# Optimization experiments

Measured on AMD Instinct MI355X. Metric: run time of the kernel, lower is better.

Reference implementation:

```python
import jax, jax.numpy as jnp
import numpy as np

N = 40000   # num nodes
C = 128     # in_channels
H = 8       # num_heads
D = C // H  # head_dim = 16
E = 640000  # num edges
FF = 4 * C


def layer_norm(x, g, b, eps=1e-5):
    m = jnp.mean(x, axis=-1, keepdims=True)
    v = jnp.mean((x - m) ** 2, axis=-1, keepdims=True)
    return (x - m) / jnp.sqrt(v + eps) * g + b


def setup_inputs() -> dict:
    key = jax.random.key(0)
    ks = jax.random.split(key, 16)
    s = 0.02
    x = jax.random.normal(ks[0], (N, C), dtype=jnp.float32)
    edge_index = jax.random.randint(ks[1], (2, E), 0, N, dtype=jnp.int64)
    return {
        'x': x,
        'edge_index': edge_index,
        'Wq': jax.random.normal(ks[2], (C, C), jnp.float32) * s,
        'bq': jnp.zeros((C,), jnp.float32),
        'Wk': jax.random.normal(ks[3], (C, C), jnp.float32) * s,
        'bk': jnp.zeros((C,), jnp.float32),
        'Wv': jax.random.normal(ks[4], (C, C), jnp.float32) * s,
        'bv': jnp.zeros((C,), jnp.float32),
        'Wo': jax.random.normal(ks[5], (C, C), jnp.float32) * s,
        'bo': jnp.zeros((C,), jnp.float32),
        'ln1_g': jnp.ones((C,), jnp.float32),
        'ln1_b': jnp.zeros((C,), jnp.float32),
        'ln2_g': jnp.ones((C,), jnp.float32),
        'ln2_b': jnp.zeros((C,), jnp.float32),
        'W1': jax.random.normal(ks[6], (C, FF), jnp.float32) * s,
        'b1': jnp.zeros((FF,), jnp.float32),
        'W2': jax.random.normal(ks[7], (FF, C), jnp.float32) * s,
        'b2': jnp.zeros((C,), jnp.float32),
    }


def reference(x, edge_index, Wq, bq, Wk, bk, Wv, bv, Wo, bo,
              ln1_g, ln1_b, ln2_g, ln2_b, W1, b1, W2, b2):
    residual = x
    xn = layer_norm(x, ln1_g, ln1_b)
    q = (xn @ Wq + bq).reshape(N, H, D)
    k = (xn @ Wk + bk).reshape(N, H, D)
    v = (xn @ Wv + bv).reshape(N, H, D)
    src, dst = edge_index[0], edge_index[1]
    # per-edge scores: [E, H]
    scores = jnp.einsum('ehd,ehd->eh', q[dst], k[src]) / jnp.sqrt(jnp.float32(D))
    # NOTE: faithful to the source — softmax over ALL edges (dim=0), not per-destination
    attn = jax.nn.softmax(scores, axis=0)[:, :, None]          # [E, H, 1]
    weighted = v[src] * attn                                   # [E, H, D]
    aggregated = jax.ops.segment_sum(weighted, dst, num_segments=N)  # [N, H, D]
    out = aggregated.reshape(N, C) @ Wo + bo
    x1 = residual + out
    residual2 = x1
    xn2 = layer_norm(x1, ln2_g, ln2_b)
    ffn = jax.nn.relu(xn2 @ W1 + b1) @ W2 + b2
    return residual2 + ffn
```

## Files before the change

kernel.cpp:

```cpp
#include <hip/hip_runtime.h>
#include <math.h>

#define NNODES 40000
#define CCH    128
#define NH     8
#define HD     16
#define NEDGE  640000
#define NBLK   157
#define FBLK   10000
#define RBLK   40
#define EBLK   625

typedef __attribute__((ext_vector_type(8))) short bf16x8;
typedef __attribute__((ext_vector_type(4))) float f32x4;
typedef __attribute__((ext_vector_type(2))) float f32x2;

__device__ inline unsigned short f2bf(float f) {
  union { float f; unsigned u; } c; c.f = f;
  unsigned r = c.u + 0x7fffu + ((c.u >> 16) & 1u);
  return (unsigned short)(r >> 16);
}
__device__ inline float bfs(unsigned short u) { union { unsigned i; float f; } c; c.i = (unsigned)u << 16; return c.f; }
__device__ inline float bflo(unsigned u) { union { unsigned i; float f; } c; c.i = u << 16; return c.f; }
__device__ inline float bfhi(unsigned u) { union { unsigned i; float f; } c; c.i = u & 0xffff0000u; return c.f; }

__device__ inline unsigned char f2fp8(float v) {
#if __has_builtin(__builtin_amdgcn_cvt_pk_fp8_f32)
  return (unsigned char)(__builtin_amdgcn_cvt_pk_fp8_f32(v, v, 0, false) & 0xff);
#else
  union { float f; unsigned u; } c; c.f = v;
  unsigned s = (c.u >> 24) & 0x80;
  int e = (int)((c.u >> 23) & 0xff) - 127;
  unsigned m = c.u & 0x7fffff;
  if (e > 8) return s | 0x7e;
  if (e >= -6) {
    unsigned q = (m + 0x80000) >> 20; unsigned ee = e + 7;
    if (q == 8) { q = 0; ee++; }
    if (ee > 15) return s | 0x7e;
    return s | (ee << 3) | q;
  }
  if (e < -10) return (unsigned char)s;
  float a = fabsf(v); unsigned q = (unsigned)(a * 512.f + 0.5f); if (q > 7) q = 7;
  return s | q;
#endif
}
__device__ inline void fp8x4d(unsigned w, float* o) {
#if __has_builtin(__builtin_amdgcn_cvt_pk_f32_fp8)
  f32x2 lo = __builtin_amdgcn_cvt_pk_f32_fp8((int)w, false);
  f32x2 hi = __builtin_amdgcn_cvt_pk_f32_fp8((int)w, true);
  o[0] = lo[0]; o[1] = lo[1]; o[2] = hi[0]; o[3] = hi[1];
#else
  #pragma unroll
  for (int i = 0; i < 4; i++) {
    unsigned b = (w >> (8 * i)) & 0xff;
    unsigned s = b >> 7, e = (b >> 3) & 15, m = b & 7;
    float v;
    if (e) { union { unsigned u; float f; } c; c.u = ((e + 120) << 23) | (m << 20); v = c.f; }
    else v = m * (1.f / 512.f);
    o[i] = s ? -v : v;
  }
#endif
}

__global__ __launch_bounds__(256) void k_wprep_all(const float* __restrict__ Wq,
                                                   const float* __restrict__ Wk,
                                                   const float* __restrict__ Wv,
                                                   const float* __restrict__ W1,
                                                   const float* __restrict__ W2,
                                                   const float* __restrict__ bq,
                                                   const float* __restrict__ bk,
                                                   const float* __restrict__ bv,
                                                   unsigned short* __restrict__ Wqkvt,
                                                   unsigned short* __restrict__ W1t,
                                                   unsigned short* __restrict__ W2t,
                                                   float* __restrict__ bqkv,
                                                   int* __restrict__ deg) {
  int g0 = blockIdx.x * 256 + threadIdx.x;
  if (g0 < NNODES) deg[g0] = 0;
  int idx = g0;
  if (idx < 16384) { int n = idx >> 7, k = idx & 127; Wqkvt[idx] = f2bf(Wq[(size_t)k * 128 + n]); return; }
  idx -= 16384;
  if (idx < 16384) { int n = idx >> 7, k = idx & 127; Wqkvt[16384 + (n << 7) + k] = f2bf(Wk[(size_t)k * 128 + n]); return; }
  idx -= 16384;
  if (idx < 16384) { int n = idx >> 7, k = idx & 127; Wqkvt[32768 + (n << 7) + k] = f2bf(Wv[(size_t)k * 128 + n]); return; }
  idx -= 16384;
  if (idx < 65536) { int n = idx >> 7, k = idx & 127; W1t[idx] = f2bf(W1[(size_t)k * 512 + n]); return; }
  idx -= 65536;
  if (idx < 65536) { int n = idx >> 9, k = idx & 511; W2t[idx] = f2bf(W2[(size_t)k * 128 + n]); return; }
  idx -= 65536;
  if (idx < 384) bqkv[idx] = idx < 128 ? bq[idx] : (idx < 256 ? bk[idx - 128] : bv[idx - 256]);
}

__global__ __launch_bounds__(256) void k_wprep_wo(const float* __restrict__ W,
                                                  const float* __restrict__ dpart,
                                                  unsigned short* __restrict__ Wt) {
  __shared__ float sinv[8];
  if (threadIdx.x < 64) {
    int h = threadIdx.x & 7;
    float s = 0.f;
    for (int r = threadIdx.x >> 3; r < RBLK; r += 8) s += dpart[r * 8 + h];
    #pragma unroll
    for (int d = 8; d < 64; d <<= 1) s += __shfl_xor(s, d);
    if (threadIdx.x < 8) sinv[h] = 1.0f / s;
  }
  __syncthreads();
  int idx = blockIdx.x * 256 + threadIdx.x;
  if (idx >= CCH * CCH) return;
  int n = idx >> 7, k = idx & 127;
  Wt[idx] = f2bf(W[(size_t)k * CCH + n] * sinv[k >> 4]);
}

template <int NT, int OUTMODE, bool LNA, bool RELU>
__global__ __launch_bounds__(256) void k_gemm128(const void* __restrict__ Ain,
                                                 const unsigned short* __restrict__ Bt,
                                                 const float* __restrict__ bias,
                                                 const float* __restrict__ lng,
                                                 const float* __restrict__ lnb,
                                                 void* __restrict__ outp) {
  __shared__ unsigned short As[64 * 128];
  __shared__ unsigned short Bs[128 * 128];
  const int tid  = threadIdx.x;
  const int row0 = blockIdx.x * 64;
  const int l    = tid & 63;
  const int w    = tid >> 6;
  const int wr   = w >> 1;
  const int wc   = w & 1;

  if (LNA) {
    const float* x = (const float*)Ain;
    int r = tid >> 2, qt = tid & 3;
    const float4* xr = (const float4*)(x + (size_t)(row0 + r) * 128 + qt * 32);
    float4 xv[8];
    float s = 0.f, ss = 0.f;
    #pragma unroll
    for (int i = 0; i < 8; i++) {
      xv[i] = xr[i];
      s  += xv[i].x + xv[i].y + xv[i].z + xv[i].w;
      ss += xv[i].x * xv[i].x + xv[i].y * xv[i].y + xv[i].z * xv[i].z + xv[i].w * xv[i].w;
    }
    s += __shfl_xor(s, 1); ss += __shfl_xor(ss, 1);
    s += __shfl_xor(s, 2); ss += __shfl_xor(ss, 2);
    float mean = s * (1.f / 128.f);
    float var  = ss * (1.f / 128.f) - mean * mean;
    float rstd = rsqrtf(var + 1e-5f);
    #pragma unroll
    for (int i = 0; i < 8; i += 2) {
      int c0 = qt * 32 + i * 4;
      float va[8] = {xv[i].x, xv[i].y, xv[i].z, xv[i].w,
                     xv[i+1].x, xv[i+1].y, xv[i+1].z, xv[i+1].w};
      unsigned short tmp[8];
      #pragma unroll
      for (int u = 0; u < 8; u++)
        tmp[u] = f2bf((va[u] - mean) * rstd * lng[c0 + u] + lnb[c0 + u]);
      int slot = c0 >> 3;
      *(uint4*)(As + r * 128 + ((slot ^ (r & 7)) * 8)) = *(uint4*)tmp;
    }
  } else {
    const unsigned short* A = (const unsigned short*)Ain;
    #pragma unroll
    for (int it = 0; it < 4; it++) {
      int idx = it * 256 + tid;
      int r = idx >> 4, sl = idx & 15;
      uint4 vv = *(const uint4*)(A + (size_t)(row0 + r) * 128 + sl * 8);
      *(uint4*)(As + r * 128 + ((sl ^ (r & 7)) * 8)) = vv;
    }
  }

  #pragma unroll
  for (int t = 0; t < NT; t++) {
    __syncthreads();
    #pragma unroll
    for (int it = 0; it < 8; it++) {
      int idx = it * 256 + tid;
      int n = idx >> 4, sl = idx & 15;
      uint4 vv = *(const uint4*)(Bt + (size_t)(t * 128 + n) * 128 + sl * 8);
      *(uint4*)(Bs + n * 128 + ((sl ^ (n & 7)) * 8)) = vv;
    }
    __syncthreads();

    f32x4 acc[2][4] = {};
    #pragma unroll
    for (int kk = 0; kk < 4; kk++) {
      int sb = kk * 4 + (l >> 4);
      bf16x8 af[2], bfr[4];
      #pragma unroll
      for (int mi = 0; mi < 2; mi++) {
        int r = wr * 32 + mi * 16 + (l & 15);
        af[mi] = *(const bf16x8*)(As + r * 128 + ((sb ^ (r & 7)) * 8));
      }
      #pragma unroll
      for (int ni = 0; ni < 4; ni++) {
        int n = wc * 64 + ni * 16 + (l & 15);
        bfr[ni] = *(const bf16x8*)(Bs + n * 128 + ((sb ^ (n & 7)) * 8));
      }
      #pragma unroll
      for (int mi = 0; mi < 2; mi++)
        #pragma unroll
        for (int ni = 0; ni < 4; ni++)
          acc[mi][ni] = __builtin_amdgcn_mfma_f32_16x16x32_bf16(af[mi], bfr[ni], acc[mi][ni], 0, 0, 0);
    }

    #pragma unroll
    for (int mi = 0; mi < 2; mi++) {
      #pragma unroll
      for (int p = 0; p < 4; p++) {
        int r = row0 + wr * 32 + mi * 16 + (l >> 4) * 4 + p;
        #pragma unroll
        for (int ni = 0; ni < 4; ni++) {
          int cc = wc * 64 + ni * 16 + (l & 15);
          int c  = t * 128 + cc;
          float val = acc[mi][ni][p] + bias[c];
          if (RELU) val = fmaxf(val, 0.f);
          if (OUTMODE == 1) {
            ((unsigned short*)outp)[(size_t)r * (NT * 128) + c] = f2bf(val);
          } else {
            char* rowb = (char*)outp + (size_t)r * 512;
            if (t == 0)      *(unsigned short*)(rowb + cc * 2) = f2bf(val);
            else if (t == 1) *(unsigned char*)(rowb + 256 + cc) = f2fp8(val);
            else             *(unsigned char*)(rowb + 384 + cc) = f2fp8(val);
          }
        }
      }
    }
  }
}

template <bool RELU, int RESMODE, int MODE>
__global__ __launch_bounds__(256) void k_mgemm(const unsigned short* __restrict__ A,
                                               const unsigned short* __restrict__ Bt,
                                               const float* __restrict__ bias,
                                               const void* __restrict__ res,
                                               void* __restrict__ outp,
                                               int K, int Nc,
                                               const float* __restrict__ lng,
                                               const float* __restrict__ lnb,
                                               void* __restrict__ outp2) {
  __shared__ unsigned short As[64 * 64];
  __shared__ unsigned short Bs[128 * 64];
  const int tid  = threadIdx.x;
  const int row0 = blockIdx.x * 64;
  const int c0   = blockIdx.y * 128;
  const int l    = tid & 63;
  const int w    = tid >> 6;
  const int wr   = w >> 1;
  const int wc   = w & 1;

  f32x4 acc[2][4] = {};

  for (int kc = 0; kc < K; kc += 64) {
    __syncthreads();
    #pragma unroll
    for (int it = 0; it < 2; it++) {
      int idx = it * 256 + tid;
      int r = idx >> 3, s = idx & 7;
      uint4 vv = *(const uint4*)(A + (size_t)(row0 + r) * K + kc + s * 8);
      *(uint4*)(As + r * 64 + ((s ^ (r & 7)) * 8)) = vv;
    }
    #pragma unroll
    for (int it = 0; it < 4; it++) {
      int idx = it * 256 + tid;
      int n = idx >> 3, s = idx & 7;
      uint4 vv = *(const uint4*)(Bt + (size_t)(c0 + n) * K + kc + s * 8);
      *(uint4*)(Bs + n * 64 + ((s ^ (n & 7)) * 8)) = vv;
    }
    __syncthreads();
    #pragma unroll
    for (int kk = 0; kk < 2; kk++) {
      int sb = kk * 4 + (l >> 4);
      bf16x8 af[2], bfr[4];
      #pragma unroll
      for (int mi = 0; mi < 2; mi++) {
        int r = wr * 32 + mi * 16 + (l & 15);
        af[mi] = *(const bf16x8*)(As + r * 64 + ((sb ^ (r & 7)) * 8));
      }
      #pragma unroll
      for (int ni = 0; ni < 4; ni++) {
        int n = wc * 64 + ni * 16 + (l & 15);
        bfr[ni] = *(const bf16x8*)(Bs + n * 64 + ((sb ^ (n & 7)) * 8));
      }
      #pragma unroll
      for (int mi = 0; mi < 2; mi++)
        #pragma unroll
        for (int ni = 0; ni < 4; ni++)
          acc[mi][ni] = __builtin_amdgcn_mfma_f32_16x16x32_bf16(af[mi], bfr[ni], acc[mi][ni], 0, 0, 0);
    }
  }

  if constexpr (MODE == 3) {
    __shared__ float lnS[64][2], lnSS[64][2], gS[128], bS[128];
    if (tid < 128) { gS[tid] = lng[tid]; bS[tid] = lnb[tid]; }
    #pragma unroll
    for (int mi = 0; mi < 2; mi++) {
      #pragma unroll
      for (int p = 0; p < 4; p++) {
        int lr = wr * 32 + mi * 16 + (l >> 4) * 4 + p;
        int r  = row0 + lr;
        float s = 0.f, ss = 0.f;
        #pragma unroll
        for (int ni = 0; ni < 4; ni++) {
          int c = wc * 64 + ni * 16 + (l & 15);
          float val = acc[mi][ni][p] + bias[c] + ((const float*)res)[(size_t)r * 128 + c];
          acc[mi][ni][p] = val;
          s += val; ss += val * val;
        }
        #pragma unroll
        for (int d = 1; d < 16; d <<= 1) { s += __shfl_xor(s, d); ss += __shfl_xor(ss, d); }
        if ((l & 15) == 0) { lnS[lr][wc] = s; lnSS[lr][wc] = ss; }
      }
    }
    __syncthreads();
    #pragma unroll
    for (int mi = 0; mi < 2; mi++) {
      #pragma unroll
      for (int p = 0; p < 4; p++) {
        int lr = wr * 32 + mi * 16 + (l >> 4) * 4 + p;
        int r  = row0 + lr;
        float m   = (lnS[lr][0] + lnS[lr][1]) * (1.f / 128.f);
        float var = (lnSS[lr][0] + lnSS[lr][1]) * (1.f / 128.f) - m * m;
        float rstd = rsqrtf(var + 1e-5f);
        #pragma unroll
        for (int ni = 0; ni < 4; ni++) {
          int c = wc * 64 + ni * 16 + (l & 15);
          float val = acc[mi][ni][p];
          ((unsigned short*)outp)[(size_t)r * 128 + c]  = f2bf(val);
          ((unsigned short*)outp2)[(size_t)r * 128 + c] = f2bf((val - m) * rstd * gS[c] + bS[c]);
        }
      }
    }
  } else {
    #pragma unroll
    for (int mi = 0; mi < 2; mi++) {
      #pragma unroll
      for (int p = 0; p < 4; p++) {
        int r = row0 + wr * 32 + mi * 16 + (l >> 4) * 4 + p;
        #pragma unroll
        for (int ni = 0; ni < 4; ni++) {
          int c = c0 + wc * 64 + ni * 16 + (l & 15);
          float val = acc[mi][ni][p] + bias[c];
          if (RESMODE == 1) val += ((const float*)res)[(size_t)r * Nc + c];
          if (RESMODE == 2) val += bfs(((const unsigned short*)res)[(size_t)r * Nc + c]);
          if (RELU) val = fmaxf(val, 0.f);
          ((float*)outp)[(size_t)r * Nc + c] = val;
        }
      }
    }
  }
}

__global__ __launch_bounds__(256) void k_histrank(const int* __restrict__ ei,
                                                  int* __restrict__ deg,
                                                  int* __restrict__ rank) {
  int base = blockIdx.x * 1024 + threadIdx.x;
  #pragma unroll
  for (int u = 0; u < 4; u++) {
    int e = base + u * 256;
    if (e < NEDGE) rank[e] = atomicAdd(&deg[ei[NEDGE + e]], 1);
  }
}

__global__ __launch_bounds__(256) void k_scan3a(const int* __restrict__ deg,
                                                int* __restrict__ bsum) {
  int i = blockIdx.x * 256 + threadIdx.x;
  int d = (i < NNODES) ? deg[i] : 0;
  #pragma unroll
  for (int s = 1; s < 64; s <<= 1) d += __shfl_xor(d, s);
  __shared__ int ws4[4];
  if ((threadIdx.x & 63) == 0) ws4[threadIdx.x >> 6] = d;
  __syncthreads();
  if (threadIdx.x == 0) bsum[blockIdx.x] = ws4[0] + ws4[1] + ws4[2] + ws4[3];
}

__global__ __launch_bounds__(256) void k_scan3c(const int* __restrict__ deg,
                                                const int* __restrict__ bsum,
                                                int* __restrict__ off) {
  const int t = threadIdx.x;
  __shared__ int ws4[4];
  __shared__ int sbase;
  {
    int lim = blockIdx.x < NBLK ? blockIdx.x : NBLK;
    int v = (t < lim) ? bsum[t] : 0;
    #pragma unroll
    for (int s = 1; s < 64; s <<= 1) v += __shfl_xor(v, s);
    if ((t & 63) == 0) ws4[t >> 6] = v;
    __syncthreads();
    if (t == 0) sbase = ws4[0] + ws4[1] + ws4[2] + ws4[3];
    __syncthreads();
  }
  int i = blockIdx.x * 256 + t;
  int d = (i < NNODES) ? deg[i] : 0;
  int lane = t & 63, wv = t >> 6;
  int incl = d;
  #pragma unroll
  for (int s = 1; s < 64; s <<= 1) { int o = __shfl_up(incl, s); if (lane >= s) incl += o; }
  __syncthreads();
  if (lane == 63) ws4[wv] = incl;
  __syncthreads();
  int base = sbase;
  for (int w2 = 0; w2 < wv; w2++) base += ws4[w2];
  int ex = base + incl - d;
  if (i < NNODES) off[i] = ex;
  if (i == 0) off[NNODES] = NEDGE;
}

__global__ __launch_bounds__(256) void k_scatter(const int* __restrict__ ei,
                                                 const int* __restrict__ off,
                                                 const int* __restrict__ rank,
                                                 int* __restrict__ srcs) {
  int base = blockIdx.x * 1024 + threadIdx.x;
  #pragma unroll
  for (int u = 0; u < 4; u++) {
    int e = base + u * 256;
    if (e < NEDGE) srcs[off[ei[NEDGE + e]] + rank[e]] = ei[e];
  }
}

__global__ __launch_bounds__(256) void k_fused(const unsigned char* __restrict__ qkv,
                                               const int* __restrict__ off,
                                               const int* __restrict__ srcs,
                                               unsigned* __restrict__ U,
                                               float* __restrict__ hpart) {
  const int wave = threadIdx.x >> 6;
  const int lane = threadIdx.x & 63;
  const int n  = blockIdx.x * 4 + wave;
  const int g  = lane >> 3;
  const int c8 = lane & 7;

  const uint4* qp = (const uint4*)(qkv + (size_t)n * 512 + c8 * 32);
  uint4 qa = qp[0], qb = qp[1];
  float qf[16];
  qf[0]=bflo(qa.x);  qf[1]=bfhi(qa.x);  qf[2]=bflo(qa.y);  qf[3]=bfhi(qa.y);
  qf[4]=bflo(qa.z);  qf[5]=bfhi(qa.z);  qf[6]=bflo(qa.w);  qf[7]=bfhi(qa.w);
  qf[8]=bflo(qb.x);  qf[9]=bfhi(qb.x);  qf[10]=bflo(qb.y); qf[11]=bfhi(qb.y);
  qf[12]=bflo(qb.z); qf[13]=bfhi(qb.z); qf[14]=bflo(qb.w); qf[15]=bfhi(qb.w);

  float acc[16];
  #pragma unroll
  for (int i = 0; i < 16; i++) acc[i] = 0.f;
  float lsum = 0.f;

  const int i0 = off[n], i1 = off[n + 1];
  if (i1 > i0) {
    int j0 = i0 + g; if (j0 >= i1) j0 = i1 - 1;
    int sA = srcs[j0];
    int sB;
    {
      int j1 = i0 + 8 + g;
      if (j1 >= i1) j1 = i1 - 1;
      sB = srcs[j1];
    }
    const uint4* kpA = (const uint4*)(qkv + (size_t)sA * 512 + 256 + c8 * 16);
    uint4 kw = kpA[0], vw = kpA[8];

    for (int jb = i0; jb < i1; jb += 8) {
      uint4 kc = kw, vc = vw;
      bool valid = jb + g < i1;
      if (jb + 8 < i1) {
        const uint4* kpB = (const uint4*)(qkv + (size_t)sB * 512 + 256 + c8 * 16);
        kw = kpB[0]; vw = kpB[8];
      }
      if (jb + 16 < i1) {
        int j2 = jb + 16 + g;
        if (j2 >= i1) j2 = i1 - 1;
        sB = srcs[j2];
      }
      float kf[16], vf[16];
      fp8x4d(kc.x, kf + 0); fp8x4d(kc.y, kf + 4); fp8x4d(kc.z, kf + 8); fp8x4d(kc.w, kf + 12);
      fp8x4d(vc.x, vf + 0); fp8x4d(vc.y, vf + 4); fp8x4d(vc.z, vf + 8); fp8x4d(vc.w, vf + 12);
      float p = 0.f;
      #pragma unroll
      for (int i = 0; i < 16; i++) p += qf[i] * kf[i];
      float w = valid ? __expf(p * 0.25f) : 0.f;
      lsum += w;
      #pragma unroll
      for (int i = 0; i < 16; i++) acc[i] += w * vf[i];
    }
  }

  #pragma unroll
  for (int d = 8; d < 64; d <<= 1) {
    #pragma unroll
    for (int i = 0; i < 16; i++) acc[i] += __shfl_xor(acc[i], d);
    lsum += __shfl_xor(lsum, d);
  }

  __shared__ float wsum[4][8];
  if (lane < 8) {
    wsum[wave][c8] = lsum;
    unsigned o[8];
    #pragma unroll
    for (int i = 0; i < 8; i++)
      o[i] = ((unsigned)f2bf(acc[2 * i + 1]) << 16) | f2bf(acc[2 * i]);
    uint4* up = (uint4*)(U + (size_t)n * 64 + c8 * 8);
    up[0] = make_uint4(o[0], o[1], o[2], o[3]);
    up[1] = make_uint4(o[4], o[5], o[6], o[7]);
  }
  __syncthreads();
  if (threadIdx.x < 8) {
    hpart[blockIdx.x * 8 + threadIdx.x] =
        wsum[0][threadIdx.x] + wsum[1][threadIdx.x] + wsum[2][threadIdx.x] + wsum[3][threadIdx.x];
  }
}

__global__ __launch_bounds__(256) void k_reduce_part(const float* __restrict__ hpart,
                                                     float* __restrict__ dpart) {
  const int t = threadIdx.x;
  const int h = t & 7;
  const int r0 = blockIdx.x * (FBLK / RBLK);
  float s = 0.f;
  for (int r = r0 + (t >> 3); r < r0 + FBLK / RBLK; r += 32) s += hpart[r * 8 + h];
  #pragma unroll
  for (int d = 8; d < 64; d <<= 1) s += __shfl_xor(s, d);
  __shared__ float ws4[4][8];
  int lane = t & 63, wv = t >> 6;
  if (lane < 8) ws4[wv][lane] = s;
  __syncthreads();
  if (t < 8) dpart[blockIdx.x * 8 + t] = ws4[0][t] + ws4[1][t] + ws4[2][t] + ws4[3][t];
}

extern "C" void kernel_launch(void* const* d_in, const int* in_sizes, int n_in,
                              void* d_out, int out_size, void* d_ws, size_t ws_size,
                              hipStream_t stream) {
  const float* x    = (const float*)d_in[0];
  const int*   ei   = (const int*)d_in[1];
  const float* Wq   = (const float*)d_in[2];
  const float* bq   = (const float*)d_in[3];
  const float* Wk   = (const float*)d_in[4];
  const float* bk   = (const float*)d_in[5];
  const float* Wv   = (const float*)d_in[6];
  const float* bv   = (const float*)d_in[7];
  const float* Wo   = (const float*)d_in[8];
  const float* bo   = (const float*)d_in[9];
  const float* ln1g = (const float*)d_in[10];
  const float* ln1b = (const float*)d_in[11];
  const float* ln2g = (const float*)d_in[12];
  const float* ln2b = (const float*)d_in[13];
  const float* W1   = (const float*)d_in[14];
  const float* b1   = (const float*)d_in[15];
  const float* W2   = (const float*)d_in[16];
  const float* b2   = (const float*)d_in[17];
  float* out = (float*)d_out;

  char* p = (char*)d_ws;
  const size_t NCb = (size_t)NNODES * CCH * 2;
  unsigned short* xn2  = (unsigned short*)p; p += NCb;
  unsigned char*  qkvb = (unsigned char*)p;  p += (size_t)NNODES * 512;
  unsigned short* agg  = (unsigned short*)p; p += NCb;
  p += NCb;
  unsigned short* x1b  = (unsigned short*)p; p += NCb;
  int* deg    = (int*)p;                     p += (size_t)NNODES * 4 + 256;
  int* off    = (int*)p;                     p += (size_t)(NNODES + 1) * 4 + 256;
  int* rank   = (int*)p;                     p += (size_t)NEDGE * 4;
  int* srcs   = (int*)p;                     p += (size_t)NEDGE * 4;
  int* bsum   = (int*)p;                     p += 256 * 4;
  float* hpart = (float*)p;                  p += (size_t)FBLK * 8 * 4;
  float* dpart = (float*)p;                  p += (size_t)RBLK * 8 * 4 + 256;
  float* bqkv  = (float*)p;                  p += 384 * 4 + 256;
  unsigned short* Wqkvt = (unsigned short*)p; p += (size_t)384 * CCH * 2;
  unsigned short* Wot   = (unsigned short*)p; p += (size_t)CCH * CCH * 2;
  unsigned short* W1t   = (unsigned short*)p; p += (size_t)CCH * 4 * CCH * 2;
  unsigned short* W2t   = (unsigned short*)p; p += (size_t)CCH * 4 * CCH * 2;
  unsigned short* ffn1 = (unsigned short*)qkvb;

  dim3 blk(256);
  dim3 gM(NNODES / 64, 1);

  k_wprep_all<<<706, blk, 0, stream>>>(Wq, Wk, Wv, W1, W2, bq, bk, bv,
                                       Wqkvt, W1t, W2t, bqkv, deg);

  k_histrank<<<EBLK, blk, 0, stream>>>(ei, deg, rank);
  k_scan3a<<<NBLK, blk, 0, stream>>>(deg, bsum);
  k_scan3c<<<NBLK, blk, 0, stream>>>(deg, bsum, off);
  k_scatter<<<EBLK, blk, 0, stream>>>(ei, off, rank, srcs);

  k_gemm128<3, 2, true, false><<<gM, blk, 0, stream>>>(x, Wqkvt, bqkv,
                                                       ln1g, ln1b, qkvb);

  k_fused<<<FBLK, blk, 0, stream>>>(qkvb, off, srcs, (unsigned*)agg, hpart);
  k_reduce_part<<<RBLK, blk, 0, stream>>>(hpart, dpart);

  k_wprep_wo<<<64, blk, 0, stream>>>(Wo, dpart, Wot);
  k_mgemm<false, 1, 3><<<gM, blk, 0, stream>>>(agg, Wot, bo, x, x1b,
                                               CCH, CCH, ln2g, ln2b, xn2);

  k_gemm128<4, 1, false, true><<<gM, blk, 0, stream>>>(xn2, W1t, b1,
                                                       nullptr, nullptr, ffn1);
  k_mgemm<false, 2, 0><<<gM, blk, 0, stream>>>(ffn1, W2t, b2, x1b, out,
                                               4 * CCH, CCH, nullptr, nullptr, nullptr);
}
```

Before: 156.5 us.

## Fuse FFN GEMMs into one kernel and fold softmax-denominator reduction into Wo prep

Adds a fused FFN kernel that computes the W1+ReLU tile into shared memory and immediately multiplies by W2 with the residual add. This avoids writing and re-reading the 40000x512 bf16 intermediate through global memory and saves a launch. The separate partial-sum reduction kernel is removed: each of the 64 Wo-prep blocks now reduces all 10000 partials itself, which repeats that work per block. The histogram and scatter kernels also handle twice as many edges per block. The fused kernel uses about 112KB of LDS with launch bounds of one block per CU, which lowers occupancy and leaves nothing to hide latency.

```diff
diff --git a/kernel.cpp b/kernel.cpp
--- a/kernel.cpp
+++ b/kernel.cpp
@@ -8,8 +8,7 @@
 #define NEDGE  640000
 #define NBLK   157
 #define FBLK   10000
-#define RBLK   40
-#define EBLK   625
+#define EBLK   313
 
 typedef __attribute__((ext_vector_type(8))) short bf16x8;
 typedef __attribute__((ext_vector_type(4))) float f32x4;
@@ -92,16 +91,21 @@
 }
 
 __global__ __launch_bounds__(256) void k_wprep_wo(const float* __restrict__ W,
-                                                  const float* __restrict__ dpart,
+                                                  const float* __restrict__ hpart,
                                                   unsigned short* __restrict__ Wt) {
   __shared__ float sinv[8];
-  if (threadIdx.x < 64) {
+  {
     int h = threadIdx.x & 7;
     float s = 0.f;
-    for (int r = threadIdx.x >> 3; r < RBLK; r += 8) s += dpart[r * 8 + h];
+    for (int r = threadIdx.x >> 3; r < FBLK; r += 32) s += hpart[r * 8 + h];
     #pragma unroll
     for (int d = 8; d < 64; d <<= 1) s += __shfl_xor(s, d);
-    if (threadIdx.x < 8) sinv[h] = 1.0f / s;
+    __shared__ float ws4[4][8];
+    int lane = threadIdx.x & 63, wv = threadIdx.x >> 6;
+    if (lane < 8) ws4[wv][lane] = s;
+    __syncthreads();
+    if (threadIdx.x < 8)
+      sinv[h] = 1.0f / (ws4[0][h] + ws4[1][h] + ws4[2][h] + ws4[3][h]);
   }
   __syncthreads();
   int idx = blockIdx.x * 256 + threadIdx.x;
@@ -220,6 +224,132 @@
             else             *(unsigned char*)(rowb + 384 + cc) = f2fp8(val);
           }
         }
+      }
+    }
+  }
+}
+
+__global__ __launch_bounds__(256, 1) void k_ffn(const unsigned short* __restrict__ xn2,
+                                                const unsigned short* __restrict__ W1t,
+                                                const unsigned short* __restrict__ W2t,
+                                                const float* __restrict__ b1,
+                                                const float* __restrict__ b2,
+                                                const unsigned short* __restrict__ x1b,
+                                                float* __restrict__ outp) {
+  __shared__ unsigned short As[64 * 128];
+  __shared__ unsigned short Fs[64 * 512];
+  __shared__ unsigned short Bs[128 * 128];
+  const int tid  = threadIdx.x;
+  const int row0 = blockIdx.x * 64;
+  const int l    = tid & 63;
+  const int w    = tid >> 6;
+  const int wr   = w >> 1;
+  const int wc   = w & 1;
+
+  #pragma unroll
+  for (int it = 0; it < 4; it++) {
+    int idx = it * 256 + tid;
+    int r = idx >> 4, sl = idx & 15;
+    uint4 vv = *(const uint4*)(xn2 + (size_t)(row0 + r) * 128 + sl * 8);
+    *(uint4*)(As + r * 128 + ((sl ^ (r & 7)) * 8)) = vv;
+  }
+
+  #pragma unroll
+  for (int t = 0; t < 4; t++) {
+    __syncthreads();
+    #pragma unroll
+    for (int it = 0; it < 8; it++) {
+      int idx = it * 256 + tid;
+      int n = idx >> 4, sl = idx & 15;
+      uint4 vv = *(const uint4*)(W1t + (size_t)(t * 128 + n) * 128 + sl * 8);
+      *(uint4*)(Bs + n * 128 + ((sl ^ (n & 7)) * 8)) = vv;
+    }
+    __syncthreads();
+
+    f32x4 acc[2][4] = {};
+    #pragma unroll
+    for (int kk = 0; kk < 4; kk++) {
+      int sb = kk * 4 + (l >> 4);
+      bf16x8 af[2], bfr[4];
+      #pragma unroll
+      for (int mi = 0; mi < 2; mi++) {
+        int r = wr * 32 + mi * 16 + (l & 15);
+        af[mi] = *(const bf16x8*)(As + r * 128 + ((sb ^ (r & 7)) * 8));
+      }
+      #pragma unroll
+      for (int ni = 0; ni < 4; ni++) {
+        int n = wc * 64 + ni * 16 + (l & 15);
+        bfr[ni] = *(const bf16x8*)(Bs + n * 128 + ((sb ^ (n & 7)) * 8));
+      }
+      #pragma unroll
+      for (int mi = 0; mi < 2; mi++)
+        #pragma unroll
+        for (int ni = 0; ni < 4; ni++)
+          acc[mi][ni] = __builtin_amdgcn_mfma_f32_16x16x32_bf16(af[mi], bfr[ni], acc[mi][ni], 0, 0, 0);
+    }
+
+    #pragma unroll
+    for (int mi = 0; mi < 2; mi++) {
+      #pragma unroll
+      for (int p = 0; p < 4; p++) {
+        int r = wr * 32 + mi * 16 + (l >> 4) * 4 + p;
+        #pragma unroll
+        for (int ni = 0; ni < 4; ni++) {
+          int cc = wc * 64 + ni * 16 + (l & 15);
+          int c  = t * 128 + cc;
+          float val = fmaxf(acc[mi][ni][p] + b1[c], 0.f);
+          int gs = c >> 3;
+          Fs[r * 512 + ((gs ^ (r & 7)) * 8) + (c & 7)] = f2bf(val);
+        }
+      }
+    }
+  }
+
+  f32x4 acc2[2][4] = {};
+  #pragma unroll
+  for (int kc = 0; kc < 8; kc++) {
+    __syncthreads();
+    #pragma unroll
+    for (int it = 0; it < 4; it++) {
+      int idx = it * 256 + tid;
+      int n = idx >> 3, sl = idx & 7;
+      uint4 vv = *(const uint4*)(W2t + (size_t)n * 512 + kc * 64 + sl * 8);
+      *(uint4*)(Bs + n * 64 + ((sl ^ (n & 7)) * 8)) = vv;
+    }
+    __syncthreads();
+    #pragma unroll
+    for (int kk = 0; kk < 2; kk++) {
+      int sb = kk * 4 + (l >> 4);
+      bf16x8 af[2], bfr[4];
+      #pragma unroll
+      for (int mi = 0; mi < 2; mi++) {
+        int r = wr * 32 + mi * 16 + (l & 15);
+        int gs = kc * 8 + sb;
+        af[mi] = *(const bf16x8*)(Fs + r * 512 + ((gs ^ (r & 7)) * 8));
+      }
+      #pragma unroll
+      for (int ni = 0; ni < 4; ni++) {
+        int n = wc * 64 + ni * 16 + (l & 15);
+        bfr[ni] = *(const bf16x8*)(Bs + n * 64 + ((sb ^ (n & 7)) * 8));
+      }
+      #pragma unroll
+      for (int mi = 0; mi < 2; mi++)
+        #pragma unroll
+        for (int ni = 0; ni < 4; ni++)
+          acc2[mi][ni] = __builtin_amdgcn_mfma_f32_16x16x32_bf16(af[mi], bfr[ni], acc2[mi][ni], 0, 0, 0);
+    }
+  }
+
+  #pragma unroll
+  for (int mi = 0; mi < 2; mi++) {
+    #pragma unroll
+    for (int p = 0; p < 4; p++) {
+      int r = row0 + wr * 32 + mi * 16 + (l >> 4) * 4 + p;
+      #pragma unroll
+      for (int ni = 0; ni < 4; ni++) {
+        int c = wc * 64 + ni * 16 + (l & 15);
+        float val = acc2[mi][ni][p] + b2[c] + bfs(x1b[(size_t)r * 128 + c]);
+        outp[(size_t)r * 128 + c] = val;
       }
     }
   }
@@ -350,9 +480,9 @@
 __global__ __launch_bounds__(256) void k_histrank(const int* __restrict__ ei,
                                                   int* __restrict__ deg,
                                                   int* __restrict__ rank) {
-  int base = blockIdx.x * 1024 + threadIdx.x;
-  #pragma unroll
-  for (int u = 0; u < 4; u++) {
+  int base = blockIdx.x * 2048 + threadIdx.x;
+  #pragma unroll
+  for (int u = 0; u < 8; u++) {
     int e = base + u * 256;
     if (e < NEDGE) rank[e] = atomicAdd(&deg[ei[NEDGE + e]], 1);
   }
@@ -406,9 +536,9 @@
                                                  const int* __restrict__ off,
                                                  const int* __restrict__ rank,
                                                  int* __restrict__ srcs) {
-  int base = blockIdx.x * 1024 + threadIdx.x;
-  #pragma unroll
-  for (int u = 0; u < 4; u++) {
+  int base = blockIdx.x * 2048 + threadIdx.x;
+  #pragma unroll
+  for (int u = 0; u < 8; u++) {
     int e = base + u * 256;
     if (e < NEDGE) srcs[off[ei[NEDGE + e]] + rank[e]] = ei[e];
   }
@@ -499,22 +629,6 @@
     hpart[blockIdx.x * 8 + threadIdx.x] =
         wsum[0][threadIdx.x] + wsum[1][threadIdx.x] + wsum[2][threadIdx.x] + wsum[3][threadIdx.x];
   }
-}
-
-__global__ __launch_bounds__(256) void k_reduce_part(const float* __restrict__ hpart,
-                                                     float* __restrict__ dpart) {
-  const int t = threadIdx.x;
-  const int h = t & 7;
-  const int r0 = blockIdx.x * (FBLK / RBLK);
-  float s = 0.f;
-  for (int r = r0 + (t >> 3); r < r0 + FBLK / RBLK; r += 32) s += hpart[r * 8 + h];
-  #pragma unroll
-  for (int d = 8; d < 64; d <<= 1) s += __shfl_xor(s, d);
-  __shared__ float ws4[4][8];
-  int lane = t & 63, wv = t >> 6;
-  if (lane < 8) ws4[wv][lane] = s;
-  __syncthreads();
-  if (t < 8) dpart[blockIdx.x * 8 + t] = ws4[0][t] + ws4[1][t] + ws4[2][t] + ws4[3][t];
 }
 
 extern "C" void kernel_launch(void* const* d_in, const int* in_sizes, int n_in,
@@ -545,7 +659,6 @@
   unsigned short* xn2  = (unsigned short*)p; p += NCb;
   unsigned char*  qkvb = (unsigned char*)p;  p += (size_t)NNODES * 512;
   unsigned short* agg  = (unsigned short*)p; p += NCb;
-  p += NCb;
   unsigned short* x1b  = (unsigned short*)p; p += NCb;
   int* deg    = (int*)p;                     p += (size_t)NNODES * 4 + 256;
   int* off    = (int*)p;                     p += (size_t)(NNODES + 1) * 4 + 256;
@@ -553,13 +666,11 @@
   int* srcs   = (int*)p;                     p += (size_t)NEDGE * 4;
   int* bsum   = (int*)p;                     p += 256 * 4;
   float* hpart = (float*)p;                  p += (size_t)FBLK * 8 * 4;
-  float* dpart = (float*)p;                  p += (size_t)RBLK * 8 * 4 + 256;
   float* bqkv  = (float*)p;                  p += 384 * 4 + 256;
   unsigned short* Wqkvt = (unsigned short*)p; p += (size_t)384 * CCH * 2;
   unsigned short* Wot   = (unsigned short*)p; p += (size_t)CCH * CCH * 2;
   unsigned short* W1t   = (unsigned short*)p; p += (size_t)CCH * 4 * CCH * 2;
   unsigned short* W2t   = (unsigned short*)p; p += (size_t)CCH * 4 * CCH * 2;
-  unsigned short* ffn1 = (unsigned short*)qkvb;
 
   dim3 blk(256);
   dim3 gM(NNODES / 64, 1);
@@ -576,14 +687,11 @@
                                                        ln1g, ln1b, qkvb);
 
   k_fused<<<FBLK, blk, 0, stream>>>(qkvb, off, srcs, (unsigned*)agg, hpart);
-  k_reduce_part<<<RBLK, blk, 0, stream>>>(hpart, dpart);
-
-  k_wprep_wo<<<64, blk, 0, stream>>>(Wo, dpart, Wot);
+
+  k_wprep_wo<<<64, blk, 0, stream>>>(Wo, hpart, Wot);
+
   k_mgemm<false, 1, 3><<<gM, blk, 0, stream>>>(agg, Wot, bo, x, x1b,
                                                CCH, CCH, ln2g, ln2b, xn2);
 
-  k_gemm128<4, 1, false, true><<<gM, blk, 0, stream>>>(xn2, W1t, b1,
-                                                       nullptr, nullptr, ffn1);
-  k_mgemm<false, 2, 0><<<gM, blk, 0, stream>>>(ffn1, W2t, b2, x1b, out,
-                                               4 * CCH, CCH, nullptr, nullptr, nullptr);
-}
+  k_ffn<<<gM, blk, 0, stream>>>(xn2, W1t, W2t, b1, b2, x1b, out);
+}
```

Result: slower. 236.7 us (+51.3%).
